# Performance work log

Hardware: AMD Instinct MI355X
Metric: run time of the kernel (lower is better)

Reference implementation:

```python
import jax, jax.numpy as jnp
import numpy as np

ENC_DIM, DEC_DIM, ATT_DIM = 2048, 512, 512
BATCH, NPIX = 256, 196


def setup_inputs() -> dict:
    key = jax.random.key(0)
    ks = jax.random.split(key, 8)
    s = lambda d: 1.0 / np.sqrt(d)
    return {
        "encoder_out": jax.random.normal(ks[0], (BATCH, NPIX, ENC_DIM), jnp.float32),
        "decoder_hidden": jax.random.normal(ks[1], (BATCH, DEC_DIM), jnp.float32),
        "W_enc": jax.random.uniform(ks[2], (ENC_DIM, ATT_DIM), jnp.float32, -s(ENC_DIM), s(ENC_DIM)),
        "b_enc": jax.random.uniform(ks[3], (ATT_DIM,), jnp.float32, -s(ENC_DIM), s(ENC_DIM)),
        "W_dec": jax.random.uniform(ks[4], (DEC_DIM, ATT_DIM), jnp.float32, -s(DEC_DIM), s(DEC_DIM)),
        "b_dec": jax.random.uniform(ks[5], (ATT_DIM,), jnp.float32, -s(DEC_DIM), s(DEC_DIM)),
        "w_full": jax.random.uniform(ks[6], (ATT_DIM,), jnp.float32, -s(ATT_DIM), s(ATT_DIM)),
        "b_full": jax.random.uniform(ks[7], (), jnp.float32, -s(ATT_DIM), s(ATT_DIM)),
    }


def reference(encoder_out, decoder_hidden, W_enc, b_enc, W_dec, b_dec, w_full, b_full):
    # att1: (B, P, A); att2: (B, 1, A)
    att1 = jnp.einsum('bpe,ea->bpa', encoder_out, W_enc) + b_enc
    att2 = (decoder_hidden @ W_dec + b_dec)[:, None, :]
    # score: (B, P) via full_att projecting A -> 1
    att = jnp.einsum('bpa,a->bp', jax.nn.relu(att1 + att2), w_full) + b_full
    alpha = jax.nn.softmax(att, axis=1)
    context = jnp.einsum('bpe,bp->be', encoder_out, alpha)
    return context, alpha
```

## Files before the change

### kernel.cpp

```cpp
#include <hip/hip_runtime.h>
#include <hip/hip_bf16.h>

#define ENC_DIM 2048
#define DEC_DIM 512
#define ATT_DIM 512
#define BATCH   256
#define NPIX    196

typedef __attribute__((ext_vector_type(8)))  short short8;
typedef __attribute__((ext_vector_type(16))) float f32x16;

typedef const __attribute__((address_space(1))) unsigned int gu32;
typedef __attribute__((address_space(3))) unsigned int lu32;

__device__ __forceinline__ short f2bf(float x) {
    unsigned u = __builtin_bit_cast(unsigned, x);
    unsigned r = (u + 0x7FFFu + ((u >> 16) & 1u)) >> 16;
    return (short)r;
}

__global__ __launch_bounds__(256) void bahdanau_prep(
    const float* __restrict__ dec_h, const float* __restrict__ W_enc,
    const float* __restrict__ b_enc, const float* __restrict__ W_dec,
    const float* __restrict__ b_dec,
    float* __restrict__ att2pb, short* __restrict__ Wpack)
{
    int blk = blockIdx.x;
    if (blk < BATCH) {
        __shared__ float hs[DEC_DIM];
        int b = blk;
        for (int i = threadIdx.x; i < DEC_DIM; i += 256) hs[i] = dec_h[b * DEC_DIM + i];
        __syncthreads();
        for (int a = threadIdx.x; a < ATT_DIM; a += 256) {
            float s = 0.f;
            #pragma unroll 8
            for (int d = 0; d < DEC_DIM; ++d) s += hs[d] * W_dec[d * ATT_DIM + a];
            att2pb[b * ATT_DIM + a] = s + b_dec[a] + b_enc[a];
        }
    } else {
        int c    = (blk - BATCH) * 256 + threadIdx.x;
        int lane = c & 63;
        int kb16 = (c >> 6) & 127;
        int nt   = c >> 13;
        int n     = nt * 32 + (lane & 31);
        int kbase = kb16 * 16 + (lane >> 5) * 8;
        short8 v;
        #pragma unroll
        for (int j = 0; j < 8; ++j) v[j] = f2bf(W_enc[(kbase + j) * ATT_DIM + n]);
        *reinterpret_cast<short8*>(Wpack + (size_t)c * 8) = v;
    }
}

__global__ __launch_bounds__(512, 4) void bahdanau_gemm(
    const float* __restrict__ enc, const float* __restrict__ w_full,
    const float* __restrict__ att2pb, const short* __restrict__ Wpack,
    float* __restrict__ spart)
{
    __shared__ __align__(16) short Bs[2][16384];
    __shared__ float red[2][128];

    const int f  = blockIdx.x;
    const int nc = (f >> 3) & 1;
    const int pp = (f >> 4) * 8 + (f & 7);
    const int b  = pp >> 1, rh = pp & 1;

    const int tid  = threadIdx.x;
    const int lane = tid & 63;
    const int wid  = tid >> 6;
    const int rt   = wid & 3;
    const int g    = wid >> 2;

    const float* encB = enc + (size_t)b * NPIX * ENC_DIM;
    int grow = rh * 128 + rt * 32 + (lane & 31);
    if (grow > NPIX - 1) grow = NPIX - 1;
    const float* aptr = encB + (size_t)grow * ENC_DIM + ((lane >> 5) << 3);

    const short8* Wc = reinterpret_cast<const short8*>(Wpack);

    f32x16 acc[4];
    #pragma unroll
    for (int t = 0; t < 4; ++t)
        #pragma unroll
        for (int r = 0; r < 16; ++r) acc[t][r] = 0.f;

    auto STAGE = [&](int buf, int kb) {
        #pragma unroll
        for (int i = 0; i < 4; ++i) {
            int idx = tid + i * 512;
            int c   = idx >> 6;
            int ln  = idx & 63;
            int nt   = nc * 8 + (c >> 2);
            int kb16 = kb * 4 + (c & 3);
            const void* gp = (const void*)(Wc + (size_t)(nt * 128 + kb16) * 64 + ln);
            void*       lp = (void*)(&Bs[buf][idx * 8]);
            __builtin_amdgcn_global_load_lds((gu32*)gp, (lu32*)lp, 16, 0, 0);
        }
    };

    STAGE(0, 0);
    for (int kb = 0; kb < ENC_DIM / 64; ++kb) {
        int cur = kb & 1;
        __syncthreads();
        if (kb < ENC_DIM / 64 - 1) STAGE(cur ^ 1, kb + 1);
        const short* Bb = &Bs[cur][0];
        #pragma unroll
        for (int kk = 0; kk < 4; ++kk) {
            const float* ap = aptr + kb * 64 + kk * 16;
            float4 f0 = *reinterpret_cast<const float4*>(ap);
            float4 f1 = *reinterpret_cast<const float4*>(ap + 4);
            short8 afr;
            afr[0] = f2bf(f0.x); afr[1] = f2bf(f0.y);
            afr[2] = f2bf(f0.z); afr[3] = f2bf(f0.w);
            afr[4] = f2bf(f1.x); afr[5] = f2bf(f1.y);
            afr[6] = f2bf(f1.z); afr[7] = f2bf(f1.w);
            #pragma unroll
            for (int t = 0; t < 4; ++t) {
                int tt = g * 4 + t;
                short8 bfr = *reinterpret_cast<const short8*>(
                    Bb + ((tt * 4 + kk) * 64 + lane) * 8);
                acc[t] = __builtin_amdgcn_mfma_f32_32x32x16_bf16(afr, bfr, acc[t], 0, 0, 0);
            }
        }
    }

    float sp[16];
    #pragma unroll
    for (int r = 0; r < 16; ++r) sp[r] = 0.f;
    #pragma unroll
    for (int t = 0; t < 4; ++t) {
        int col  = nc * 256 + g * 128 + t * 32 + (lane & 31);
        float c2 = att2pb[b * ATT_DIM + col];
        float wf = w_full[col];
        #pragma unroll
        for (int r = 0; r < 16; ++r) {
            float v = acc[t][r] + c2;
            v = v > 0.f ? v : 0.f;
            sp[r] += v * wf;
        }
    }
    #pragma unroll
    for (int r = 0; r < 16; ++r) {
        float v = sp[r];
        v += __shfl_xor(v, 1);
        v += __shfl_xor(v, 2);
        v += __shfl_xor(v, 4);
        v += __shfl_xor(v, 8);
        v += __shfl_xor(v, 16);
        sp[r] = v;
    }
    if ((lane & 31) == 0) {
        #pragma unroll
        for (int r = 0; r < 16; ++r) {
            int lr = rt * 32 + (r & 3) + 8 * (r >> 2) + 4 * (lane >> 5);
            red[g][lr] = sp[r];
        }
    }
    __syncthreads();
    if (tid < 128) {
        int p = rh * 128 + tid;
        if (p < NPIX)
            spart[nc * (BATCH * 224) + b * 224 + p] = red[0][tid] + red[1][tid];
    }
}

__global__ __launch_bounds__(512) void bahdanau_ctx(
    const float* __restrict__ enc, const float* __restrict__ spart,
    float* __restrict__ out_ctx, float* __restrict__ out_alpha)
{
    __shared__ float al[256];
    __shared__ float msum[2];
    const int b    = blockIdx.x;
    const int tid  = threadIdx.x;
    const int lane = tid & 63;
    const int wid  = tid >> 6;

    if (tid < NPIX)
        al[tid] = spart[b * 224 + tid] + spart[BATCH * 224 + b * 224 + tid];
    else if (tid < 256)
        al[tid] = -3.4e38f;
    __syncthreads();

    if (wid == 0) {
        float s0 = al[lane], s1 = al[lane + 64], s2 = al[lane + 128], s3 = al[lane + 192];
        float m = fmaxf(fmaxf(s0, s1), fmaxf(s2, s3));
        #pragma unroll
        for (int d = 1; d <= 32; d <<= 1) m = fmaxf(m, __shfl_xor(m, d));
        float e = __expf(s0 - m) + __expf(s1 - m) + __expf(s2 - m) + __expf(s3 - m);
        #pragma unroll
        for (int d = 1; d <= 32; d <<= 1) e += __shfl_xor(e, d);
        if (lane == 0) { msum[0] = m; msum[1] = e; }
    }
    __syncthreads();
    float m    = msum[0];
    float rinv = 1.f / msum[1];
    if (tid < NPIX) {
        float a = __expf(al[tid] - m) * rinv;
        al[tid] = a;
        out_alpha[b * NPIX + tid] = a;
    }
    __syncthreads();

    float4 c4 = {0.f, 0.f, 0.f, 0.f};
    const float4* enc4 = reinterpret_cast<const float4*>(enc + (size_t)b * NPIX * ENC_DIM);
    #pragma unroll 4
    for (int p = 0; p < NPIX; ++p) {
        float a  = al[p];
        float4 v = enc4[(size_t)p * (ENC_DIM / 4) + tid];
        c4.x += a * v.x; c4.y += a * v.y; c4.z += a * v.z; c4.w += a * v.w;
    }
    reinterpret_cast<float4*>(out_ctx)[(size_t)b * (ENC_DIM / 4) + tid] = c4;
}

extern "C" void kernel_launch(void* const* d_in, const int* in_sizes, int n_in,
                              void* d_out, int out_size, void* d_ws, size_t ws_size,
                              hipStream_t stream) {
    const float* enc    = (const float*)d_in[0];
    const float* dech   = (const float*)d_in[1];
    const float* W_enc  = (const float*)d_in[2];
    const float* b_enc  = (const float*)d_in[3];
    const float* W_dec  = (const float*)d_in[4];
    const float* b_dec  = (const float*)d_in[5];
    const float* w_full = (const float*)d_in[6];

    float* att2pb = (float*)d_ws;
    short* Wpack  = (short*)((char*)d_ws + 512 * 1024);
    float* spart  = (float*)((char*)d_ws + 2560 * 1024);

    float* out_ctx   = (float*)d_out;
    float* out_alpha = out_ctx + (size_t)BATCH * ENC_DIM;

    bahdanau_prep<<<768, 256, 0, stream>>>(dech, W_enc, b_enc, W_dec, b_dec, att2pb, Wpack);
    bahdanau_gemm<<<1024, 512, 0, stream>>>(enc, w_full, att2pb, Wpack, spart);
    bahdanau_ctx<<<BATCH, 512, 0, stream>>>(enc, spart, out_ctx, out_alpha);
}
```

Baseline: 447.9 us.

## Flatten GEMM over batch*pixels, stage A through LDS with triple buffering

The attention GEMM now tiles the flattened (batch*pixel) rows in 128-row tiles, which removes the padding waste of per-batch 256-row tiles (784 workgroups instead of 1024). The encoder tile is converted to bf16 once and written into LDS, replacing per-wave direct global loads, and waves use a 2x2 MFMA block that shares A and B fragments. A three-buffer pipeline with explicit waitcnt and barriers overlaps the loads with compute, and MFMA sections raise wave priority. In exchange, LDS use and register pressure per workgroup go up (launch bounds lowered to 2), and the epilogue needs a per-row division to find each row's batch index for att2.

```diff
diff --git a/kernel.cpp b/kernel.cpp
--- a/kernel.cpp
+++ b/kernel.cpp
@@ -6,6 +6,8 @@
 #define ATT_DIM 512
 #define BATCH   256
 #define NPIX    196
+#define MROWS   (BATCH * NPIX)
+#define NTILES  64
 
 typedef __attribute__((ext_vector_type(8)))  short short8;
 typedef __attribute__((ext_vector_type(16))) float f32x16;
@@ -51,116 +53,146 @@
     }
 }
 
-__global__ __launch_bounds__(512, 4) void bahdanau_gemm(
+__global__ __launch_bounds__(512, 2) void bahdanau_gemm(
     const float* __restrict__ enc, const float* __restrict__ w_full,
     const float* __restrict__ att2pb, const short* __restrict__ Wpack,
     float* __restrict__ spart)
 {
-    __shared__ __align__(16) short Bs[2][16384];
-    __shared__ float red[2][128];
-
-    const int f  = blockIdx.x;
-    const int nc = (f >> 3) & 1;
-    const int pp = (f >> 4) * 8 + (f & 7);
-    const int b  = pp >> 1, rh = pp & 1;
+    __shared__ __align__(16) short lds_s[3 * 12288];
+    __shared__ float redm[4][128];
+
+    const int wg  = blockIdx.x;
+    const int swz = (wg & 7) * 98 + (wg >> 3);
+    const int mt  = swz >> 1;
+    const int nc  = swz & 1;
 
     const int tid  = threadIdx.x;
     const int lane = tid & 63;
     const int wid  = tid >> 6;
-    const int rt   = wid & 3;
-    const int g    = wid >> 2;
-
-    const float* encB = enc + (size_t)b * NPIX * ENC_DIM;
-    int grow = rh * 128 + rt * 32 + (lane & 31);
-    if (grow > NPIX - 1) grow = NPIX - 1;
-    const float* aptr = encB + (size_t)grow * ENC_DIM + ((lane >> 5) << 3);
-
-    const short8* Wc = reinterpret_cast<const short8*>(Wpack);
-
-    f32x16 acc[4];
-    #pragma unroll
-    for (int t = 0; t < 4; ++t)
-        #pragma unroll
-        for (int r = 0; r < 16; ++r) acc[t][r] = 0.f;
-
-    auto STAGE = [&](int buf, int kb) {
-        #pragma unroll
-        for (int i = 0; i < 4; ++i) {
-            int idx = tid + i * 512;
-            int c   = idx >> 6;
-            int ln  = idx & 63;
-            int nt   = nc * 8 + (c >> 2);
-            int kb16 = kb * 4 + (c & 3);
-            const void* gp = (const void*)(Wc + (size_t)(nt * 128 + kb16) * 64 + ln);
-            void*       lp = (void*)(&Bs[buf][idx * 8]);
-            __builtin_amdgcn_global_load_lds((gu32*)gp, (lu32*)lp, 16, 0, 0);
-        }
+    const int wm   = wid >> 2;
+    const int wn   = wid & 3;
+
+    const int ca    = tid;
+    const int arow  = ((ca >> 7) << 5) + (ca & 31);
+    const int akoff = (((ca >> 6) & 1) << 4) + (((ca >> 5) & 1) << 3);
+    const float* aSrc = enc + (size_t)(mt * 128 + arow) * ENC_DIM + akoff;
+    short* aDst = lds_s + ca * 8;
+
+    const int cb0 = tid, cb1 = tid + 512;
+    const short* bg0 = Wpack + (size_t)(((nc * 8 + (cb0 >> 7)) * 128 + ((cb0 >> 6) & 1)) * 64 + (cb0 & 63)) * 8;
+    const short* bg1 = Wpack + (size_t)(((nc * 8 + (cb1 >> 7)) * 128 + ((cb1 >> 6) & 1)) * 64 + (cb1 & 63)) * 8;
+
+    f32x16 acc[2][2];
+    #pragma unroll
+    for (int i = 0; i < 2; ++i)
+        #pragma unroll
+        for (int j = 0; j < 2; ++j)
+            #pragma unroll
+            for (int r = 0; r < 16; ++r) acc[i][j][r] = 0.f;
+
+    auto stageB = [&](int t, int buf) {
+        short* lb = lds_s + buf * 12288 + 4096;
+        __builtin_amdgcn_global_load_lds((gu32*)(bg0 + (size_t)t * 1024),
+                                         (lu32*)(lb + cb0 * 8), 16, 0, 0);
+        __builtin_amdgcn_global_load_lds((gu32*)(bg1 + (size_t)t * 1024),
+                                         (lu32*)(lb + cb1 * 8), 16, 0, 0);
     };
-
-    STAGE(0, 0);
-    for (int kb = 0; kb < ENC_DIM / 64; ++kb) {
-        int cur = kb & 1;
-        __syncthreads();
-        if (kb < ENC_DIM / 64 - 1) STAGE(cur ^ 1, kb + 1);
-        const short* Bb = &Bs[cur][0];
-        #pragma unroll
-        for (int kk = 0; kk < 4; ++kk) {
-            const float* ap = aptr + kb * 64 + kk * 16;
-            float4 f0 = *reinterpret_cast<const float4*>(ap);
-            float4 f1 = *reinterpret_cast<const float4*>(ap + 4);
-            short8 afr;
-            afr[0] = f2bf(f0.x); afr[1] = f2bf(f0.y);
-            afr[2] = f2bf(f0.z); afr[3] = f2bf(f0.w);
-            afr[4] = f2bf(f1.x); afr[5] = f2bf(f1.y);
-            afr[6] = f2bf(f1.z); afr[7] = f2bf(f1.w);
+    auto writeA = [&](int buf, float4 v0, float4 v1) {
+        short8 w;
+        w[0] = f2bf(v0.x); w[1] = f2bf(v0.y); w[2] = f2bf(v0.z); w[3] = f2bf(v0.w);
+        w[4] = f2bf(v1.x); w[5] = f2bf(v1.y); w[6] = f2bf(v1.z); w[7] = f2bf(v1.w);
+        *reinterpret_cast<short8*>(aDst + buf * 12288) = w;
+    };
+
+    float4 a0, a1;
+    {
+        const float4* p0 = reinterpret_cast<const float4*>(aSrc);
+        float4 t0 = p0[0], t1 = p0[1];
+        stageB(0, 0);
+        const float4* p1 = reinterpret_cast<const float4*>(aSrc + 32);
+        a0 = p1[0]; a1 = p1[1];
+        stageB(1, 1);
+        writeA(0, t0, t1);
+        asm volatile("s_waitcnt vmcnt(4) lgkmcnt(0)" ::: "memory");
+        __builtin_amdgcn_s_barrier();
+    }
+
+    int bc = 0, bn = 1, bn2 = 2;
+    for (int t = 0; t < NTILES; ++t) {
+        if (t < NTILES - 1) writeA(bn, a0, a1);
+        if (t < NTILES - 2) {
+            const float4* p = reinterpret_cast<const float4*>(aSrc + (t + 2) * 32);
+            a0 = p[0]; a1 = p[1];
+            stageB(t + 2, bn2);
+        }
+        {
+            const short* bA = lds_s + bc * 12288;
+            const short* bB = bA + 4096;
             #pragma unroll
-            for (int t = 0; t < 4; ++t) {
-                int tt = g * 4 + t;
-                short8 bfr = *reinterpret_cast<const short8*>(
-                    Bb + ((tt * 4 + kk) * 64 + lane) * 8);
-                acc[t] = __builtin_amdgcn_mfma_f32_32x32x16_bf16(afr, bfr, acc[t], 0, 0, 0);
+            for (int kk = 0; kk < 2; ++kk) {
+                short8 af0 = *reinterpret_cast<const short8*>(bA + (((wm * 2 + 0) * 2 + kk) * 64 + lane) * 8);
+                short8 af1 = *reinterpret_cast<const short8*>(bA + (((wm * 2 + 1) * 2 + kk) * 64 + lane) * 8);
+                short8 bf0 = *reinterpret_cast<const short8*>(bB + (((wn * 2 + 0) * 2 + kk) * 64 + lane) * 8);
+                short8 bf1 = *reinterpret_cast<const short8*>(bB + (((wn * 2 + 1) * 2 + kk) * 64 + lane) * 8);
+                __builtin_amdgcn_s_setprio(1);
+                acc[0][0] = __builtin_amdgcn_mfma_f32_32x32x16_bf16(af0, bf0, acc[0][0], 0, 0, 0);
+                acc[0][1] = __builtin_amdgcn_mfma_f32_32x32x16_bf16(af0, bf1, acc[0][1], 0, 0, 0);
+                acc[1][0] = __builtin_amdgcn_mfma_f32_32x32x16_bf16(af1, bf0, acc[1][0], 0, 0, 0);
+                acc[1][1] = __builtin_amdgcn_mfma_f32_32x32x16_bf16(af1, bf1, acc[1][1], 0, 0, 0);
+                __builtin_amdgcn_s_setprio(0);
             }
         }
-    }
-
-    float sp[16];
-    #pragma unroll
-    for (int r = 0; r < 16; ++r) sp[r] = 0.f;
-    #pragma unroll
-    for (int t = 0; t < 4; ++t) {
-        int col  = nc * 256 + g * 128 + t * 32 + (lane & 31);
-        float c2 = att2pb[b * ATT_DIM + col];
+        if (t < NTILES - 1) {
+            if (t < NTILES - 2)
+                asm volatile("s_waitcnt vmcnt(4) lgkmcnt(0)" ::: "memory");
+            else
+                asm volatile("s_waitcnt vmcnt(0) lgkmcnt(0)" ::: "memory");
+            __builtin_amdgcn_s_barrier();
+        }
+        int tmp = bc; bc = bn; bn = bn2; bn2 = tmp;
+    }
+
+    float sp0[16], sp1[16];
+    #pragma unroll
+    for (int r = 0; r < 16; ++r) { sp0[r] = 0.f; sp1[r] = 0.f; }
+    #pragma unroll
+    for (int j = 0; j < 2; ++j) {
+        int col  = nc * 256 + (wn * 2 + j) * 32 + (lane & 31);
         float wf = w_full[col];
+        const float* a2 = att2pb + col;
         #pragma unroll
         for (int r = 0; r < 16; ++r) {
-            float v = acc[t][r] + c2;
-            v = v > 0.f ? v : 0.f;
-            sp[r] += v * wf;
+            int rit  = (r & 3) + 8 * (r >> 2) + 4 * (lane >> 5);
+            int row0 = mt * 128 + (wm * 2 + 0) * 32 + rit;
+            int row1 = row0 + 32;
+            float v0 = acc[0][j][r] + a2[(row0 / NPIX) * ATT_DIM];
+            float v1 = acc[1][j][r] + a2[(row1 / NPIX) * ATT_DIM];
+            sp0[r] += fmaxf(v0, 0.f) * wf;
+            sp1[r] += fmaxf(v1, 0.f) * wf;
         }
     }
     #pragma unroll
     for (int r = 0; r < 16; ++r) {
-        float v = sp[r];
-        v += __shfl_xor(v, 1);
-        v += __shfl_xor(v, 2);
-        v += __shfl_xor(v, 4);
-        v += __shfl_xor(v, 8);
-        v += __shfl_xor(v, 16);
-        sp[r] = v;
+        float v0 = sp0[r], v1 = sp1[r];
+        #pragma unroll
+        for (int d = 1; d <= 16; d <<= 1) {
+            v0 += __shfl_xor(v0, d);
+            v1 += __shfl_xor(v1, d);
+        }
+        sp0[r] = v0; sp1[r] = v1;
     }
     if ((lane & 31) == 0) {
         #pragma unroll
         for (int r = 0; r < 16; ++r) {
-            int lr = rt * 32 + (r & 3) + 8 * (r >> 2) + 4 * (lane >> 5);
-            red[g][lr] = sp[r];
-        }
-    }
-    __syncthreads();
-    if (tid < 128) {
-        int p = rh * 128 + tid;
-        if (p < NPIX)
-            spart[nc * (BATCH * 224) + b * 224 + p] = red[0][tid] + red[1][tid];
-    }
+            int rit = (r & 3) + 8 * (r >> 2) + 4 * (lane >> 5);
+            redm[wn][(wm * 2 + 0) * 32 + rit] = sp0[r];
+            redm[wn][(wm * 2 + 1) * 32 + rit] = sp1[r];
+        }
+    }
+    __syncthreads();
+    if (tid < 128)
+        spart[(size_t)nc * MROWS + mt * 128 + tid] =
+            redm[0][tid] + redm[1][tid] + redm[2][tid] + redm[3][tid];
 }
 
 __global__ __launch_bounds__(512) void bahdanau_ctx(
@@ -174,10 +206,12 @@
     const int lane = tid & 63;
     const int wid  = tid >> 6;
 
-    if (tid < NPIX)
-        al[tid] = spart[b * 224 + tid] + spart[BATCH * 224 + b * 224 + tid];
-    else if (tid < 256)
+    if (tid < NPIX) {
+        int row = b * NPIX + tid;
+        al[tid] = spart[row] + spart[MROWS + row];
+    } else if (tid < 256) {
         al[tid] = -3.4e38f;
+    }
     __syncthreads();
 
     if (wid == 0) {
@@ -230,6 +264,6 @@
     float* out_alpha = out_ctx + (size_t)BATCH * ENC_DIM;
 
     bahdanau_prep<<<768, 256, 0, stream>>>(dech, W_enc, b_enc, W_dec, b_dec, att2pb, Wpack);
-    bahdanau_gemm<<<1024, 512, 0, stream>>>(enc, w_full, att2pb, Wpack, spart);
+    bahdanau_gemm<<<784, 512, 0, stream>>>(enc, w_full, att2pb, Wpack, spart);
     bahdanau_ctx<<<BATCH, 512, 0, stream>>>(enc, spart, out_ctx, out_alpha);
 }
```

Result: slower. 488.9 us (+9.1%).

## Retile GEMM over flattened rows with LDS-staged A tiles and 16x16 MFMA

Applied to the files above, without the earlier changes.

The score GEMM now treats all batch×pixel rows as one flat M dimension of 128-row tiles, split four ways over N, so the padded per-batch 224-row tiles go away. Both the fp32 encoder tile (XOR-swizzled) and the packed bf16 weights are staged into LDS with async global_load_lds and double buffering. Conversion uses the packed v_cvt_pk_bf16_f32 instruction and the MFMA becomes 16x16x32. The cost is per-row batch lookups for att2 and four partial score arrays to sum, and spart is laid out over 50176 rows (four N-chunks) where it was 224 padded slots per batch.

```diff
diff --git a/kernel.cpp b/kernel.cpp
--- a/kernel.cpp
+++ b/kernel.cpp
@@ -6,9 +6,11 @@
 #define ATT_DIM 512
 #define BATCH   256
 #define NPIX    196
+#define MROWS   (BATCH * NPIX)
+#define KT_N    64
 
 typedef __attribute__((ext_vector_type(8)))  short short8;
-typedef __attribute__((ext_vector_type(16))) float f32x16;
+typedef __attribute__((ext_vector_type(4)))  float f32x4;
 
 typedef const __attribute__((address_space(1))) unsigned int gu32;
 typedef __attribute__((address_space(3))) unsigned int lu32;
@@ -17,6 +19,11 @@
     unsigned u = __builtin_bit_cast(unsigned, x);
     unsigned r = (u + 0x7FFFu + ((u >> 16) & 1u)) >> 16;
     return (short)r;
+}
+__device__ __forceinline__ unsigned pkbf(float a, float b) {
+    unsigned r;
+    asm("v_cvt_pk_bf16_f32 %0, %1, %2" : "=v"(r) : "v"(a), "v"(b));
+    return r;
 }
 
 __global__ __launch_bounds__(256) void bahdanau_prep(
@@ -38,12 +45,12 @@
             att2pb[b * ATT_DIM + a] = s + b_dec[a] + b_enc[a];
         }
     } else {
-        int c    = (blk - BATCH) * 256 + threadIdx.x;
-        int lane = c & 63;
-        int kb16 = (c >> 6) & 127;
-        int nt   = c >> 13;
-        int n     = nt * 32 + (lane & 31);
-        int kbase = kb16 * 16 + (lane >> 5) * 8;
+        int c  = (blk - BATCH) * 256 + threadIdx.x;
+        int l  = c & 63;
+        int kt = (c >> 6) & 63;
+        int nt = c >> 12;
+        int n     = nt * 16 + (l & 15);
+        int kbase = kt * 32 + ((l >> 4) & 3) * 8;
         short8 v;
         #pragma unroll
         for (int j = 0; j < 8; ++j) v[j] = f2bf(W_enc[(kbase + j) * ATT_DIM + n]);
@@ -51,116 +58,131 @@
     }
 }
 
-__global__ __launch_bounds__(512, 4) void bahdanau_gemm(
+__global__ __launch_bounds__(256) void bahdanau_gemm(
     const float* __restrict__ enc, const float* __restrict__ w_full,
     const float* __restrict__ att2pb, const short* __restrict__ Wpack,
     float* __restrict__ spart)
 {
-    __shared__ __align__(16) short Bs[2][16384];
-    __shared__ float red[2][128];
-
-    const int f  = blockIdx.x;
-    const int nc = (f >> 3) & 1;
-    const int pp = (f >> 4) * 8 + (f & 7);
-    const int b  = pp >> 1, rh = pp & 1;
+    __shared__ __align__(16) char lds[2 * 24576];
+    __shared__ float redm[2][128];
+
+    const int wg = blockIdx.x;
+    const int mt = ((wg >> 5) << 3) | (wg & 7);
+    const int nc = (wg >> 3) & 3;
 
     const int tid  = threadIdx.x;
     const int lane = tid & 63;
     const int wid  = tid >> 6;
-    const int rt   = wid & 3;
-    const int g    = wid >> 2;
-
-    const float* encB = enc + (size_t)b * NPIX * ENC_DIM;
-    int grow = rh * 128 + rt * 32 + (lane & 31);
-    if (grow > NPIX - 1) grow = NPIX - 1;
-    const float* aptr = encB + (size_t)grow * ENC_DIM + ((lane >> 5) << 3);
-
-    const short8* Wc = reinterpret_cast<const short8*>(Wpack);
-
-    f32x16 acc[4];
-    #pragma unroll
-    for (int t = 0; t < 4; ++t)
-        #pragma unroll
-        for (int r = 0; r < 16; ++r) acc[t][r] = 0.f;
-
-    auto STAGE = [&](int buf, int kb) {
-        #pragma unroll
-        for (int i = 0; i < 4; ++i) {
-            int idx = tid + i * 512;
-            int c   = idx >> 6;
-            int ln  = idx & 63;
-            int nt   = nc * 8 + (c >> 2);
-            int kb16 = kb * 4 + (c & 3);
-            const void* gp = (const void*)(Wc + (size_t)(nt * 128 + kb16) * 64 + ln);
-            void*       lp = (void*)(&Bs[buf][idx * 8]);
-            __builtin_amdgcn_global_load_lds((gu32*)gp, (lu32*)lp, 16, 0, 0);
+    const int wm   = wid >> 1;
+    const int wn   = wid & 1;
+
+    size_t aoff[4];
+    #pragma unroll
+    for (int s = 0; s < 4; ++s) {
+        int i = tid + 256 * s, r = i >> 3, qq = i & 7;
+        aoff[s] = (size_t)(mt * 128 + r) * ENC_DIM + ((qq ^ (r & 7)) << 2);
+    }
+    size_t boff[2];
+    #pragma unroll
+    for (int s = 0; s < 2; ++s) {
+        int i = tid + 256 * s, f = i >> 6, ln = i & 63;
+        boff[s] = ((size_t)(nc * 8 + f) * 64 * 64 + ln) * 8;
+    }
+
+    f32x4 acc[4][4];
+    #pragma unroll
+    for (int a = 0; a < 4; ++a)
+        #pragma unroll
+        for (int c = 0; c < 4; ++c)
+            #pragma unroll
+            for (int r = 0; r < 4; ++r) acc[a][c][r] = 0.f;
+
+    auto STAGE = [&](int buf, int kt) {
+        char* ab = lds + buf * 24576;
+        char* bb = ab + 16384;
+        #pragma unroll
+        for (int s = 0; s < 4; ++s)
+            __builtin_amdgcn_global_load_lds((gu32*)(enc + aoff[s] + kt * 32),
+                                             (lu32*)(ab + (tid + 256 * s) * 16), 16, 0, 0);
+        #pragma unroll
+        for (int s = 0; s < 2; ++s)
+            __builtin_amdgcn_global_load_lds((gu32*)(Wpack + boff[s] + (size_t)kt * 512),
+                                             (lu32*)(bb + (tid + 256 * s) * 16), 16, 0, 0);
+    };
+
+    auto COMPUTE = [&](int buf) {
+        const char* ab = lds + buf * 24576;
+        const char* bb = ab + 16384;
+        short8 af[4], bf[4];
+        #pragma unroll
+        for (int rt = 0; rt < 4; ++rt) {
+            int r  = wm * 64 + rt * 16 + (lane & 15);
+            int q0 = ((lane >> 4) & 3) * 2;
+            float4 lo = *reinterpret_cast<const float4*>(ab + r * 128 + ((q0       ^ (r & 7)) << 4));
+            float4 hi = *reinterpret_cast<const float4*>(ab + r * 128 + (((q0 + 1) ^ (r & 7)) << 4));
+            union { short8 s; unsigned u[4]; } fr;
+            fr.u[0] = pkbf(lo.x, lo.y); fr.u[1] = pkbf(lo.z, lo.w);
+            fr.u[2] = pkbf(hi.x, hi.y); fr.u[3] = pkbf(hi.z, hi.w);
+            af[rt] = fr.s;
         }
+        #pragma unroll
+        for (int ct = 0; ct < 4; ++ct)
+            bf[ct] = *reinterpret_cast<const short8*>(bb + (wn * 4 + ct) * 1024 + lane * 16);
+        #pragma unroll
+        for (int rt = 0; rt < 4; ++rt)
+            #pragma unroll
+            for (int ct = 0; ct < 4; ++ct)
+                acc[rt][ct] = __builtin_amdgcn_mfma_f32_16x16x32_bf16(af[rt], bf[ct], acc[rt][ct], 0, 0, 0);
     };
 
     STAGE(0, 0);
-    for (int kb = 0; kb < ENC_DIM / 64; ++kb) {
-        int cur = kb & 1;
+    __syncthreads();
+    for (int kt2 = 0; kt2 < KT_N; kt2 += 2) {
+        STAGE(1, kt2 + 1);
+        COMPUTE(0);
         __syncthreads();
-        if (kb < ENC_DIM / 64 - 1) STAGE(cur ^ 1, kb + 1);
-        const short* Bb = &Bs[cur][0];
-        #pragma unroll
-        for (int kk = 0; kk < 4; ++kk) {
-            const float* ap = aptr + kb * 64 + kk * 16;
-            float4 f0 = *reinterpret_cast<const float4*>(ap);
-            float4 f1 = *reinterpret_cast<const float4*>(ap + 4);
-            short8 afr;
-            afr[0] = f2bf(f0.x); afr[1] = f2bf(f0.y);
-            afr[2] = f2bf(f0.z); afr[3] = f2bf(f0.w);
-            afr[4] = f2bf(f1.x); afr[5] = f2bf(f1.y);
-            afr[6] = f2bf(f1.z); afr[7] = f2bf(f1.w);
-            #pragma unroll
-            for (int t = 0; t < 4; ++t) {
-                int tt = g * 4 + t;
-                short8 bfr = *reinterpret_cast<const short8*>(
-                    Bb + ((tt * 4 + kk) * 64 + lane) * 8);
-                acc[t] = __builtin_amdgcn_mfma_f32_32x32x16_bf16(afr, bfr, acc[t], 0, 0, 0);
+        if (kt2 + 2 < KT_N) STAGE(0, kt2 + 2);
+        COMPUTE(1);
+        __syncthreads();
+    }
+
+    float srow[16];
+    #pragma unroll
+    for (int i = 0; i < 16; ++i) srow[i] = 0.f;
+    #pragma unroll
+    for (int ct = 0; ct < 4; ++ct) {
+        int col  = nc * 128 + wn * 64 + ct * 16 + (lane & 15);
+        float wf = w_full[col];
+        #pragma unroll
+        for (int rt = 0; rt < 4; ++rt) {
+            #pragma unroll
+            for (int r = 0; r < 4; ++r) {
+                unsigned grow = mt * 128 + wm * 64 + rt * 16 + ((lane >> 4) & 3) * 4 + r;
+                unsigned bb   = grow / NPIX;
+                float v = acc[rt][ct][r] + att2pb[bb * ATT_DIM + col];
+                srow[rt * 4 + r] += fmaxf(v, 0.f) * wf;
             }
         }
     }
-
-    float sp[16];
-    #pragma unroll
-    for (int r = 0; r < 16; ++r) sp[r] = 0.f;
-    #pragma unroll
-    for (int t = 0; t < 4; ++t) {
-        int col  = nc * 256 + g * 128 + t * 32 + (lane & 31);
-        float c2 = att2pb[b * ATT_DIM + col];
-        float wf = w_full[col];
-        #pragma unroll
-        for (int r = 0; r < 16; ++r) {
-            float v = acc[t][r] + c2;
-            v = v > 0.f ? v : 0.f;
-            sp[r] += v * wf;
-        }
-    }
-    #pragma unroll
-    for (int r = 0; r < 16; ++r) {
-        float v = sp[r];
+    #pragma unroll
+    for (int i = 0; i < 16; ++i) {
+        float v = srow[i];
         v += __shfl_xor(v, 1);
         v += __shfl_xor(v, 2);
         v += __shfl_xor(v, 4);
         v += __shfl_xor(v, 8);
-        v += __shfl_xor(v, 16);
-        sp[r] = v;
-    }
-    if ((lane & 31) == 0) {
-        #pragma unroll
-        for (int r = 0; r < 16; ++r) {
-            int lr = rt * 32 + (r & 3) + 8 * (r >> 2) + 4 * (lane >> 5);
-            red[g][lr] = sp[r];
-        }
-    }
-    __syncthreads();
-    if (tid < 128) {
-        int p = rh * 128 + tid;
-        if (p < NPIX)
-            spart[nc * (BATCH * 224) + b * 224 + p] = red[0][tid] + red[1][tid];
-    }
+        srow[i] = v;
+    }
+    if ((lane & 15) == 0) {
+        #pragma unroll
+        for (int rt = 0; rt < 4; ++rt)
+            #pragma unroll
+            for (int r = 0; r < 4; ++r)
+                redm[wn][wm * 64 + rt * 16 + ((lane >> 4) & 3) * 4 + r] = srow[rt * 4 + r];
+    }
+    __syncthreads();
+    if (tid < 128)
+        spart[(size_t)nc * MROWS + mt * 128 + tid] = redm[0][tid] + redm[1][tid];
 }
 
 __global__ __launch_bounds__(512) void bahdanau_ctx(
@@ -174,10 +196,12 @@
     const int lane = tid & 63;
     const int wid  = tid >> 6;
 
-    if (tid < NPIX)
-        al[tid] = spart[b * 224 + tid] + spart[BATCH * 224 + b * 224 + tid];
-    else if (tid < 256)
+    if (tid < NPIX) {
+        int row = b * NPIX + tid;
+        al[tid] = spart[row] + spart[MROWS + row] + spart[2 * MROWS + row] + spart[3 * MROWS + row];
+    } else if (tid < 256) {
         al[tid] = -3.4e38f;
+    }
     __syncthreads();
 
     if (wid == 0) {
@@ -230,6 +254,6 @@
     float* out_alpha = out_ctx + (size_t)BATCH * ENC_DIM;
 
     bahdanau_prep<<<768, 256, 0, stream>>>(dech, W_enc, b_enc, W_dec, b_dec, att2pb, Wpack);
-    bahdanau_gemm<<<1024, 512, 0, stream>>>(enc, w_full, att2pb, Wpack, spart);
+    bahdanau_gemm<<<1568, 256, 0, stream>>>(enc, w_full, att2pb, Wpack, spart);
     bahdanau_ctx<<<BATCH, 512, 0, stream>>>(enc, spart, out_ctx, out_alpha);
 }
```

After: 425.8 us. -4.9%, faster.
